# Optimization experiments

Measured on AMD Instinct MI355X. Metric: run time of the kernel, lower is better.

Reference implementation:

```python
import jax, jax.numpy as jnp
import numpy as np

N_MESH = 40962  # icosahedral level-6 mesh nodes (x[..., -40962:])


def _lin_coords(out_size, in_size, scale):
    # torch F.interpolate bilinear, align_corners=False source coords
    i = jnp.arange(out_size, dtype=jnp.float32)
    src = jnp.maximum((i + 0.5) / scale - 0.5, 0.0)
    i0 = jnp.clip(jnp.floor(src).astype(jnp.int32), 0, in_size - 1)
    i1 = jnp.minimum(i0 + 1, in_size - 1)
    w = src - i0.astype(jnp.float32)
    return i0, i1, w


def _bilinear4(x):
    # x: (B,C,H,W) -> (B,C,4H,4W), separable bilinear, align_corners=False
    B, C, H, W = x.shape
    i0, i1, wh = _lin_coords(4 * H, H, 4.0)
    x = x[:, :, i0, :] * (1.0 - wh)[None, None, :, None] + x[:, :, i1, :] * wh[None, None, :, None]
    j0, j1, ww = _lin_coords(4 * W, W, 4.0)
    x = x[:, :, :, j0] * (1.0 - ww) + x[:, :, :, j1] * ww
    return x


def _grid2mesh(x, lat, lon):
    # x: (B,C,H,W); drop last lat row, upsample x4, append broadcast pole row
    B, C, H, W = x.shape
    pole = x[:, :, -1, 0][:, :, None, None] * jnp.ones((B, C, 1, 4 * W), x.dtype)
    xi = _bilinear4(x[:, :, :-1, :])            # (B,C,4(H-1),4W)
    xi = jnp.concatenate([xi, pole], axis=2)    # (B,C,4(H-1)+1,4W)
    return xi[:, :, lat - 1, lon - 1]           # (B,C,M) gather at mesh coords


def _gcn(h, W, b, src, dst, norm, n):
    # GCNConv: sym-normalized scatter-add aggregation of linearly transformed feats
    h = h @ W                                    # (B,N,Hd)
    msg = lambda hb: jax.ops.segment_sum(hb[src] * norm[:, None], dst, num_segments=n)
    return jax.vmap(msg)(h) + b


def reference(x, edge_index, Lat, Lon, W1, b1, W2, b2, Wl, bl, Wl1, bl1):
    B, C, H, Wd = x.shape
    mesh = _grid2mesh(x, Lat, Lon)                               # (B,C,M)
    feats = jnp.concatenate([x.reshape(B, C, H * Wd), mesh], -1)  # (B,C,N)
    h = feats.transpose(0, 2, 1)                                 # (B,N,C)
    n = h.shape[1]

    # gcn_norm with self loops (edge_weight = 1)
    loops = jnp.arange(n, dtype=edge_index.dtype)
    src = jnp.concatenate([edge_index[0], loops])
    dst = jnp.concatenate([edge_index[1], loops])
    deg = jax.ops.segment_sum(jnp.ones(src.shape, h.dtype), dst, num_segments=n)
    dinv = jnp.where(deg > 0, deg ** -0.5, 0.0)
    norm = dinv[src] * dinv[dst]

    h = _gcn(h, W1, b1, src, dst, norm, n)
    h = jax.nn.gelu(h, approximate=False)
    h = _gcn(h, W2, b2, src, dst, norm, n)
    h = h[:, -N_MESH:, :]                                        # keep mesh nodes
    out = jax.nn.gelu((h @ Wl + bl) @ Wl1 + bl1, approximate=False)
    return out.transpose(0, 2, 1)                                # (B,out_ch,M)


def setup_inputs() -> dict:
    key = jax.random.key(0)
    ks = jax.random.split(key, 16)
    B, C, H, W = 1, 69, 181, 360
    HID, OUT = 256, 256
    N = H * W + N_MESH  # 106122
    E = 500000
    x = jax.random.normal(ks[0], (B, C, H, W), jnp.float32)
    edge_index = jax.random.randint(ks[1], (2, E), 0, N, dtype=jnp.int64)
    Lat = jax.random.randint(ks[2], (N_MESH,), 1, 4 * (H - 1) + 2, dtype=jnp.int64)
    Lon = jax.random.randint(ks[3], (N_MESH,), 1, 4 * W + 1, dtype=jnp.int64)
    s = 0.05
    return {
        "x": x, "edge_index": edge_index, "Lat": Lat, "Lon": Lon,
        "W1": jax.random.normal(ks[4], (C, HID), jnp.float32) * s,
        "b1": jnp.zeros((HID,), jnp.float32),
        "W2": jax.random.normal(ks[5], (HID, HID), jnp.float32) * s,
        "b2": jnp.zeros((HID,), jnp.float32),
        "Wl": jax.random.normal(ks[6], (HID, 256), jnp.float32) * s,
        "bl": jnp.zeros((256,), jnp.float32),
        "Wl1": jax.random.normal(ks[7], (256, OUT), jnp.float32) * s,
        "bl1": jnp.zeros((OUT,), jnp.float32),
    }
```

## Files before the change

### kernel.cpp

```cpp
#include <hip/hip_runtime.h>

#define NGRID 65160
#define NMESH 40962
#define NTOT  (NGRID + NMESH)
#define CIN   69
#define KPAD1 96
#define HID   256
#define HH    181
#define WWID  360
#define SCAN_BS 1024
#define NBLK_SCAN ((NTOT + SCAN_BS - 1) / SCAN_BS)

#define NT1TILES ((NTOT + 63) / 64)
#define NT1PAD   (NT1TILES * 64)
#define NT2TILES ((NMESH + 63) / 64)
#define NT2PAD   (NT2TILES * 64)

#define W1OFF  0
#define WCOFF  (96 * 256)
#define WALLK  (96 + 256)

typedef float f32x4 __attribute__((ext_vector_type(4)));
typedef _Float16 f16;
typedef _Float16 f16x2 __attribute__((ext_vector_type(2)));
typedef _Float16 f16x4 __attribute__((ext_vector_type(4)));
typedef _Float16 f16x8 __attribute__((ext_vector_type(8)));

__device__ __forceinline__ float gelu_exact(float v) {
    return 0.5f * v * (1.0f + erff(v * 0.7071067811865476f));
}

__global__ __launch_bounds__(256) void transpose_x(const float* __restrict__ x,
                                                   f16* __restrict__ h0g) {
    __shared__ float tile[96][65];
    int s0 = blockIdx.x * 64;
    int t = threadIdx.x;
#pragma unroll
    for (int i = 0; i < 24; ++i) {
        int idx = t + i * 256;
        int c = idx >> 6, s = idx & 63;
        int gs = s0 + s;
        float v = 0.f;
        if (c < CIN && gs < NGRID) v = x[(size_t)c * NGRID + gs];
        tile[c][s] = v;
    }
    __syncthreads();
#pragma unroll
    for (int i = 0; i < 12; ++i) {
        int idx = t + i * 256;
        int r = idx / 48, u = idx % 48;
        int gr = s0 + r;
        if (gr < NGRID) {
            f16x2 p;
            p.x = (f16)tile[u * 2 + 0][r];
            p.y = (f16)tile[u * 2 + 1][r];
            ((f16x2*)h0g)[(size_t)gr * 48 + u] = p;
        }
    }
}

__global__ __launch_bounds__(256) void mesh_interp(const f16* __restrict__ h0g,
                                                   const int* __restrict__ Lat,
                                                   const int* __restrict__ Lon,
                                                   f16* __restrict__ h0m) {
    int t = blockIdx.x * 256 + threadIdx.x;
    if (t >= NMESH * 48) return;
    int j = t / 48, u = t % 48;
    int la = Lat[j] - 1;
    int lo = Lon[j] - 1;
    const f16x2* g = (const f16x2*)h0g;
    f16x2 o;
    if (la == 720) {
        o = g[(size_t)(180 * WWID) * 48 + u];
    } else {
        float sh = fmaxf((la + 0.5f) * 0.25f - 0.5f, 0.0f);
        int i0 = min((int)sh, HH - 2);
        int i1 = min(i0 + 1, HH - 2);
        float wh = sh - (float)i0;
        float sw = fmaxf((lo + 0.5f) * 0.25f - 0.5f, 0.0f);
        int j0 = min((int)sw, WWID - 1);
        int j1 = min(j0 + 1, WWID - 1);
        float ww = sw - (float)j0;
        f16x2 v00 = g[(size_t)(i0 * WWID + j0) * 48 + u];
        f16x2 v10 = g[(size_t)(i1 * WWID + j0) * 48 + u];
        f16x2 v01 = g[(size_t)(i0 * WWID + j1) * 48 + u];
        f16x2 v11 = g[(size_t)(i1 * WWID + j1) * 48 + u];
        float ax = (float)v00.x + ((float)v10.x - (float)v00.x) * wh;
        float ay = (float)v00.y + ((float)v10.y - (float)v00.y) * wh;
        float bx = (float)v01.x + ((float)v11.x - (float)v01.x) * wh;
        float by = (float)v01.y + ((float)v11.y - (float)v01.y) * wh;
        o.x = (f16)(ax + (bx - ax) * ww);
        o.y = (f16)(ay + (by - ay) * ww);
    }
    ((f16x2*)h0m)[(size_t)j * 48 + u] = o;
}

__global__ void deg_init(float* __restrict__ deg, int* __restrict__ cnt) {
    int i = blockIdx.x * 256 + threadIdx.x;
    if (i < NTOT) { deg[i] = 1.0f; cnt[i] = 0; }
}
__global__ void deg_scatter(const int* __restrict__ ei, float* __restrict__ deg, int E) {
    int e = blockIdx.x * 256 + threadIdx.x;
    if (e < E) atomicAdd(&deg[ei[E + e]], 1.0f);
}

__global__ __launch_bounds__(SCAN_BS) void scan1(const float* __restrict__ deg,
                                                 float* __restrict__ dinv,
                                                 int* __restrict__ off, int* __restrict__ bsum) {
    __shared__ int s[SCAN_BS];
    int t = threadIdx.x;
    int i = blockIdx.x * SCAN_BS + t;
    int v = (i < NTOT) ? ((int)deg[i] - 1) : 0;
    if (i < NTOT) dinv[i] = 1.0f / sqrtf((float)(v + 1));
    s[t] = v; __syncthreads();
    for (int d = 1; d < SCAN_BS; d <<= 1) {
        int x = (t >= d) ? s[t - d] : 0;
        __syncthreads();
        s[t] += x;
        __syncthreads();
    }
    if (i < NTOT) off[i] = s[t] - v;
    if (t == SCAN_BS - 1) bsum[blockIdx.x] = s[t];
}
__global__ void scan2(int* __restrict__ bsum) {
    __shared__ int s[128];
    int t = threadIdx.x;
    int v = (t < NBLK_SCAN) ? bsum[t] : 0;
    s[t] = v; __syncthreads();
    for (int d = 1; d < 128; d <<= 1) {
        int x = (t >= d) ? s[t - d] : 0;
        __syncthreads();
        s[t] += x;
        __syncthreads();
    }
    if (t < NBLK_SCAN) bsum[t] = s[t] - v;
}
__global__ __launch_bounds__(SCAN_BS) void scan3(int* __restrict__ off, const int* __restrict__ bsum) {
    int i = blockIdx.x * SCAN_BS + threadIdx.x;
    if (i < NTOT) off[i] += bsum[blockIdx.x];
}

__global__ void csr_fill(const int* __restrict__ ei, const float* __restrict__ dinv,
                         const int* __restrict__ off, int* __restrict__ cnt,
                         int2* __restrict__ epk, int E) {
    int e = blockIdx.x * 256 + threadIdx.x;
    if (e >= E) return;
    int s = ei[e], d = ei[E + e];
    int pos = off[d] + atomicAdd(&cnt[d], 1);
    epk[pos] = make_int2(s, __float_as_int(dinv[s] * dinv[d]));
}

__global__ __launch_bounds__(256) void wgemm(const float* __restrict__ A,
                                             const float* __restrict__ B,
                                             float* __restrict__ C) {
    __shared__ float As[16][68];
    __shared__ float Bs[16][64];
    int r0 = blockIdx.y * 64, c0 = blockIdx.x * 64;
    int t = threadIdx.x;
    int tr = t >> 4, tc = t & 15;
    float acc[4][4] = {};
    for (int kk = 0; kk < 256; kk += 16) {
#pragma unroll
        for (int i = 0; i < 4; ++i) {
            int idx = t + i * 256;
            int r = idx >> 4, k = idx & 15;
            As[k][r] = A[(size_t)(r0 + r) * 256 + kk + k];
        }
#pragma unroll
        for (int i = 0; i < 4; ++i) {
            int idx = t + i * 256;
            int k = idx >> 6, c = idx & 63;
            Bs[k][c] = B[(size_t)(kk + k) * 256 + c0 + c];
        }
        __syncthreads();
#pragma unroll
        for (int k = 0; k < 16; ++k) {
            float a[4], b[4];
#pragma unroll
            for (int i = 0; i < 4; ++i) a[i] = As[k][tr * 4 + i];
#pragma unroll
            for (int j = 0; j < 4; ++j) b[j] = Bs[k][tc * 4 + j];
#pragma unroll
            for (int i = 0; i < 4; ++i)
#pragma unroll
                for (int j = 0; j < 4; ++j) acc[i][j] = fmaf(a[i], b[j], acc[i][j]);
        }
        __syncthreads();
    }
#pragma unroll
    for (int i = 0; i < 4; ++i)
#pragma unroll
        for (int j = 0; j < 4; ++j)
            C[(size_t)(r0 + tr * 4 + i) * 256 + c0 + tc * 4 + j] = acc[i][j];
}

__global__ __launch_bounds__(256) void bias_k(const float* __restrict__ b2,
                                              const float* __restrict__ M1,
                                              const float* __restrict__ bl,
                                              const float* __restrict__ Wl1,
                                              const float* __restrict__ bl1,
                                              float* __restrict__ bc) {
    int c = threadIdx.x;
    float acc = bl1[c];
    for (int j = 0; j < 256; ++j) {
        acc = fmaf(b2[j], M1[(size_t)j * 256 + c], acc);
        acc = fmaf(bl[j], Wl1[(size_t)j * 256 + c], acc);
    }
    bc[c] = acc;
}

__global__ void pack_f16(const float* __restrict__ W1, const float* __restrict__ Wc,
                         f16* __restrict__ wp) {
    int t = blockIdx.x * 256 + threadIdx.x;
    if (t >= WALLK * HID) return;
    int kg = t >> 8, c = t & 255;
    const float* src; int k, Kw; size_t base;
    if (kg < 96) { src = W1; k = kg;      Kw = CIN; base = W1OFF; }
    else         { src = Wc; k = kg - 96; Kw = HID; base = WCOFF; }
    float v = (k < Kw) ? src[(size_t)k * HID + c] : 0.f;
    size_t idx = base + ((((size_t)(k >> 3)) * HID + c) << 3) + (k & 7);
    wp[idx] = (f16)v;
}

__global__ __launch_bounds__(256) void agg1(const f16* __restrict__ h0,
                                            const float* __restrict__ deg,
                                            const float* __restrict__ dinv,
                                            const int* __restrict__ off,
                                            const int2* __restrict__ epk,
                                            f16* __restrict__ P0) {
    int wv = (blockIdx.x * 256 + threadIdx.x) >> 6;
    if (wv >= NT1PAD) return;
    int lane = threadIdx.x & 63;
    if (lane >= 48) return;
    int r = wv & 63, tile = wv >> 6;
    char* dst = (char*)P0 + (size_t)tile * 12288 + ((r * 192 + lane * 4) ^ ((r & 7) << 4));
    if (wv >= NTOT) { *(unsigned*)dst = 0u; return; }
    int d = wv;
    const f16x2* g = (const f16x2*)h0;
    float dv = dinv[d];
    float w2 = dv * dv;
    f16x2 v = g[(size_t)d * 48 + lane];
    float ax = w2 * (float)v.x;
    float ay = w2 * (float)v.y;
    const int2* ep = epk + off[d];
    int n = (int)deg[d] - 1;
    int p = 0;
    for (; p + 4 <= n; p += 4) {
        int2 e0 = ep[p], e1 = ep[p + 1], e2 = ep[p + 2], e3 = ep[p + 3];
        f16x2 u0 = g[(size_t)e0.x * 48 + lane];
        f16x2 u1 = g[(size_t)e1.x * 48 + lane];
        f16x2 u2 = g[(size_t)e2.x * 48 + lane];
        f16x2 u3 = g[(size_t)e3.x * 48 + lane];
        float w0 = __int_as_float(e0.y), w1 = __int_as_float(e1.y);
        float w2b = __int_as_float(e2.y), w3 = __int_as_float(e3.y);
        ax = fmaf(w0, (float)u0.x, ax); ay = fmaf(w0, (float)u0.y, ay);
        ax = fmaf(w1, (float)u1.x, ax); ay = fmaf(w1, (float)u1.y, ay);
        ax = fmaf(w2b, (float)u2.x, ax); ay = fmaf(w2b, (float)u2.y, ay);
        ax = fmaf(w3, (float)u3.x, ax); ay = fmaf(w3, (float)u3.y, ay);
    }
    for (; p < n; ++p) {
        int2 e = ep[p];
        f16x2 u = g[(size_t)e.x * 48 + lane];
        float w = __int_as_float(e.y);
        ax = fmaf(w, (float)u.x, ax);
        ay = fmaf(w, (float)u.y, ay);
    }
    f16x2 o; o.x = (f16)ax; o.y = (f16)ay;
    *(f16x2*)dst = o;
}

__global__ __launch_bounds__(256) void agg2(const f16* __restrict__ A,
                                            const float* __restrict__ deg,
                                            const float* __restrict__ dinv,
                                            const int* __restrict__ off,
                                            const int2* __restrict__ epk,
                                            f16* __restrict__ P2) {
    int wv = (blockIdx.x * 256 + threadIdx.x) >> 6;
    if (wv >= NT2PAD) return;
    int lane = threadIdx.x & 63;
    int r = wv & 63, tile = wv >> 6;
    char* dst = (char*)P2 + (size_t)tile * 32768 + ((r * 512 + lane * 8) ^ ((r & 7) << 4));
    if (wv >= NMESH) { *(unsigned long long*)dst = 0ull; return; }
    int d = NGRID + wv;
    const f16x4* g = (const f16x4*)A;
    float dv = dinv[d];
    float w2 = dv * dv;
    f16x4 v = g[(size_t)d * 64 + lane];
    float4 acc;
    acc.x = w2 * (float)v.x; acc.y = w2 * (float)v.y;
    acc.z = w2 * (float)v.z; acc.w = w2 * (float)v.w;
    const int2* ep = epk + off[d];
    int n = (int)deg[d] - 1;
    int p = 0;
    for (; p + 4 <= n; p += 4) {
        int2 e0 = ep[p], e1 = ep[p + 1], e2 = ep[p + 2], e3 = ep[p + 3];
        f16x4 u0 = g[(size_t)e0.x * 64 + lane];
        f16x4 u1 = g[(size_t)e1.x * 64 + lane];
        f16x4 u2 = g[(size_t)e2.x * 64 + lane];
        f16x4 u3 = g[(size_t)e3.x * 64 + lane];
        float w0 = __int_as_float(e0.y), w1 = __int_as_float(e1.y);
        float w2b = __int_as_float(e2.y), w3 = __int_as_float(e3.y);
        acc.x = fmaf(w0, (float)u0.x, acc.x); acc.y = fmaf(w0, (float)u0.y, acc.y);
        acc.z = fmaf(w0, (float)u0.z, acc.z); acc.w = fmaf(w0, (float)u0.w, acc.w);
        acc.x = fmaf(w1, (float)u1.x, acc.x); acc.y = fmaf(w1, (float)u1.y, acc.y);
        acc.z = fmaf(w1, (float)u1.z, acc.z); acc.w = fmaf(w1, (float)u1.w, acc.w);
        acc.x = fmaf(w2b, (float)u2.x, acc.x); acc.y = fmaf(w2b, (float)u2.y, acc.y);
        acc.z = fmaf(w2b, (float)u2.z, acc.z); acc.w = fmaf(w2b, (float)u2.w, acc.w);
        acc.x = fmaf(w3, (float)u3.x, acc.x); acc.y = fmaf(w3, (float)u3.y, acc.y);
        acc.z = fmaf(w3, (float)u3.z, acc.z); acc.w = fmaf(w3, (float)u3.w, acc.w);
    }
    for (; p < n; ++p) {
        int2 e = ep[p];
        f16x4 u = g[(size_t)e.x * 64 + lane];
        float w = __int_as_float(e.y);
        acc.x = fmaf(w, (float)u.x, acc.x); acc.y = fmaf(w, (float)u.y, acc.y);
        acc.z = fmaf(w, (float)u.z, acc.z); acc.w = fmaf(w, (float)u.w, acc.w);
    }
    f16x4 o;
    o.x = (f16)acc.x; o.y = (f16)acc.y; o.z = (f16)acc.z; o.w = (f16)acc.w;
    *(f16x4*)dst = o;
}

__global__ __launch_bounds__(256) void gemm1_f16(const f16* __restrict__ P0,
                                                 const f16* __restrict__ wp,
                                                 const float* __restrict__ bias,
                                                 f16* __restrict__ Af) {
    __shared__ __align__(16) f16 As[64 * 96];
    const int tile = blockIdx.x;
    const int row0 = tile * 64;
    const int t = threadIdx.x;
    const int lane = t & 63;
    const int wave = t >> 6;
    const int l15 = lane & 15, l4 = lane >> 4;
    const int colw = wave * 64;
    const char* src = (const char*)P0 + (size_t)tile * 12288;
#pragma unroll
    for (int i = 0; i < 3; ++i) {
        int o = t * 16 + i * 4096;
        *(uint4*)((char*)As + o) = *(const uint4*)(src + o);
    }
    __syncthreads();
    f32x4 acc[4][4] = {};
#pragma unroll
    for (int ks = 0; ks < 96; ks += 32) {
        f16x8 a[4], b[4];
#pragma unroll
        for (int rb = 0; rb < 4; ++rb) {
            int r = rb * 16 + l15;
            int byte = r * 192 + (ks + l4 * 8) * 2;
            int swz = byte ^ ((r & 7) << 4);
            a[rb] = *(f16x8*)((char*)As + swz);
        }
#pragma unroll
        for (int cb = 0; cb < 4; ++cb) {
            int c = colw + cb * 16 + l15;
            size_t off = ((((size_t)ks >> 3) + l4) * HID + c) << 3;
            b[cb] = *(const f16x8*)(wp + W1OFF + off);
        }
#pragma unroll
        for (int rb = 0; rb < 4; ++rb)
#pragma unroll
            for (int cb = 0; cb < 4; ++cb)
                acc[rb][cb] = __builtin_amdgcn_mfma_f32_16x16x32_f16(a[rb], b[cb], acc[rb][cb], 0, 0, 0);
    }
#pragma unroll
    for (int rb = 0; rb < 4; ++rb) {
#pragma unroll
        for (int r = 0; r < 4; ++r) {
            int gr = row0 + rb * 16 + l4 * 4 + r;
            if (gr < NTOT) {
#pragma unroll
                for (int cb = 0; cb < 4; ++cb) {
                    int gc = colw + cb * 16 + l15;
                    float v = acc[rb][cb][r] + bias[gc];
                    Af[(size_t)gr * HID + gc] = (f16)gelu_exact(v);
                }
            }
        }
    }
}

__global__ __launch_bounds__(256) void final_k(const f16* __restrict__ P2,
                                               const f16* __restrict__ wp,
                                               const float* __restrict__ bc,
                                               float* __restrict__ out) {
    __shared__ __align__(16) f16 Ps[64 * 256];
    const int tile = blockIdx.x;
    const int row0 = tile * 64;
    const int t = threadIdx.x;
    const int lane = t & 63;
    const int wave = t >> 6;
    const int l15 = lane & 15, l4 = lane >> 4;
    const int cw = wave * 64;
    const char* src = (const char*)P2 + (size_t)tile * 32768;
#pragma unroll
    for (int i = 0; i < 8; ++i) {
        int o = t * 16 + i * 4096;
        *(uint4*)((char*)Ps + o) = *(const uint4*)(src + o);
    }
    __syncthreads();
    f32x4 acc[4][4] = {};
#pragma unroll
    for (int ks = 0; ks < 256; ks += 32) {
        f16x8 w[4], p[4];
#pragma unroll
        for (int mb = 0; mb < 4; ++mb) {
            int c = cw + mb * 16 + l15;
            size_t off = ((((size_t)ks >> 3) + l4) * HID + c) << 3;
            w[mb] = *(const f16x8*)(wp + WCOFF + off);
        }
#pragma unroll
        for (int jb = 0; jb < 4; ++jb) {
            int r = jb * 16 + l15;
            int byte = r * 512 + (ks + l4 * 8) * 2;
            int swz = byte ^ ((r & 7) << 4);
            p[jb] = *(f16x8*)((char*)Ps + swz);
        }
#pragma unroll
        for (int mb = 0; mb < 4; ++mb)
#pragma unroll
            for (int jb = 0; jb < 4; ++jb)
                acc[mb][jb] = __builtin_amdgcn_mfma_f32_16x16x32_f16(w[mb], p[jb], acc[mb][jb], 0, 0, 0);
    }
    const bool full = (row0 + 64 <= NMESH);
#pragma unroll
    for (int mb = 0; mb < 4; ++mb) {
#pragma unroll
        for (int r = 0; r < 4; ++r) {
            int c = cw + mb * 16 + l4 * 4 + r;
            float bv = bc[c];
            float* orow = out + (size_t)c * NMESH + row0;
#pragma unroll
            for (int jb = 0; jb < 4; ++jb) {
                int j = jb * 16 + l15;
                float v = gelu_exact(acc[mb][jb][r] + bv);
                if (full || row0 + j < NMESH) orow[j] = v;
            }
        }
    }
}

extern "C" void kernel_launch(void* const* d_in, const int* in_sizes, int n_in,
                              void* d_out, int out_size, void* d_ws, size_t ws_size,
                              hipStream_t stream) {
    const float* x   = (const float*)d_in[0];
    const int*   ei  = (const int*)d_in[1];
    const int*   Lat = (const int*)d_in[2];
    const int*   Lon = (const int*)d_in[3];
    const float* W1  = (const float*)d_in[4];
    const float* b1  = (const float*)d_in[5];
    const float* W2  = (const float*)d_in[6];
    const float* b2  = (const float*)d_in[7];
    const float* Wl  = (const float*)d_in[8];
    const float* bl  = (const float*)d_in[9];
    const float* Wl1 = (const float*)d_in[10];
    const float* bl1 = (const float*)d_in[11];
    float* out = (float*)d_out;
    const int E = in_sizes[1] / 2;

    f16*   h0  = (f16*)d_out;
    int2*  epk = (int2*)((char*)d_out + (size_t)NTOT * KPAD1 * 2);

    f16*   P0   = (f16*)d_ws;
    f16*   Af   = P0 + (size_t)NT1TILES * 6144;
    f16*   P2   = Af + (size_t)NTOT * HID;
    float* deg  = (float*)(P2 + (size_t)NT2TILES * 16384);
    float* dinv = deg + NTOT;
    int*   off  = (int*)(dinv + NTOT);
    int*   cnt  = off + NTOT;
    int*   bsum = cnt + NTOT;
    float* M1   = (float*)(bsum + 128);
    float* WcF  = M1 + HID * HID;
    float* bc   = WcF + HID * HID;
    f16*   wp   = (f16*)(bc + HID);

    transpose_x<<<(NGRID + 63) / 64, 256, 0, stream>>>(x, h0);
    mesh_interp<<<(NMESH * 48 + 255) / 256, 256, 0, stream>>>(h0, Lat, Lon,
                                                              h0 + (size_t)NGRID * KPAD1);

    deg_init<<<(NTOT + 255) / 256, 256, 0, stream>>>(deg, cnt);
    deg_scatter<<<(E + 255) / 256, 256, 0, stream>>>(ei, deg, E);
    scan1<<<NBLK_SCAN, SCAN_BS, 0, stream>>>(deg, dinv, off, bsum);
    scan2<<<1, 128, 0, stream>>>(bsum);
    scan3<<<NBLK_SCAN, SCAN_BS, 0, stream>>>(off, bsum);
    csr_fill<<<(E + 255) / 256, 256, 0, stream>>>(ei, dinv, off, cnt, epk, E);

    dim3 gW(4, 4);
    wgemm<<<gW, 256, 0, stream>>>(Wl, Wl1, M1);
    wgemm<<<gW, 256, 0, stream>>>(W2, M1, WcF);
    bias_k<<<1, 256, 0, stream>>>(b2, M1, bl, Wl1, bl1, bc);
    pack_f16<<<(WALLK * HID + 255) / 256, 256, 0, stream>>>(W1, WcF, wp);

    agg1<<<(int)(((long long)NT1PAD * 64 + 255) / 256), 256, 0, stream>>>(
        h0, deg, dinv, off, epk, P0);
    gemm1_f16<<<NT1TILES, 256, 0, stream>>>(P0, wp, b1, Af);

    agg2<<<(int)(((long long)NT2PAD * 64 + 255) / 256), 256, 0, stream>>>(
        Af, deg, dinv, off, epk, P2);

    final_k<<<NT2TILES, 256, 0, stream>>>(P2, wp, bc, out);
}
```

Baseline: 257.2 us.

## Vectorize hidden-layer stores and stage final output through LDS for coalesced writes

The first GEMM epilogue now packs four f16 outputs per lane into one vector store. This permutes the column order of the intermediate features, and the packed Wc weight rows are permuted to match. The final kernel no longer writes strided scalar outputs. It stages GELU results in padded LDS in two channel halves, then writes coalesced float4 rows of the channel-major output. This adds extra barriers and LDS traffic, and the float4 stores rely on dword-aligned (not 16-byte aligned) global addresses since NMESH is not a multiple of 4.

```diff
diff --git a/kernel.cpp b/kernel.cpp
--- a/kernel.cpp
+++ b/kernel.cpp
@@ -214,11 +214,17 @@
     int t = blockIdx.x * 256 + threadIdx.x;
     if (t >= WALLK * HID) return;
     int kg = t >> 8, c = t & 255;
-    const float* src; int k, Kw; size_t base;
-    if (kg < 96) { src = W1; k = kg;      Kw = CIN; base = W1OFF; }
-    else         { src = Wc; k = kg - 96; Kw = HID; base = WCOFF; }
-    float v = (k < Kw) ? src[(size_t)k * HID + c] : 0.f;
-    size_t idx = base + ((((size_t)(k >> 3)) * HID + c) << 3) + (k & 7);
+    float v;
+    size_t idx;
+    if (kg < 96) {
+        v = (kg < CIN) ? W1[(size_t)kg * HID + c] : 0.f;
+        idx = W1OFF + ((((size_t)(kg >> 3)) * HID + c) << 3) + (kg & 7);
+    } else {
+        int ks = kg - 96;
+        int kl = (ks & ~63) + ((ks & 3) << 4) + ((ks & 63) >> 2);
+        v = Wc[(size_t)kl * HID + c];
+        idx = WCOFF + ((((size_t)(ks >> 3)) * HID + c) << 3) + (ks & 7);
+    }
     wp[idx] = (f16)v;
 }
 
@@ -369,12 +375,14 @@
         for (int r = 0; r < 4; ++r) {
             int gr = row0 + rb * 16 + l4 * 4 + r;
             if (gr < NTOT) {
+                f16x4 o;
 #pragma unroll
                 for (int cb = 0; cb < 4; ++cb) {
                     int gc = colw + cb * 16 + l15;
                     float v = acc[rb][cb][r] + bias[gc];
-                    Af[(size_t)gr * HID + gc] = (f16)gelu_exact(v);
+                    o[cb] = (f16)gelu_exact(v);
                 }
+                *(f16x4*)(Af + (size_t)gr * HID + colw + l15 * 4) = o;
             }
         }
     }
@@ -384,7 +392,9 @@
                                                const f16* __restrict__ wp,
                                                const float* __restrict__ bc,
                                                float* __restrict__ out) {
-    __shared__ __align__(16) f16 Ps[64 * 256];
+    __shared__ __align__(16) char smem[64 * 132 * 4];
+    f16* Ps = (f16*)smem;
+    float* lf = (float*)smem;
     const int tile = blockIdx.x;
     const int row0 = tile * 64;
     const int t = threadIdx.x;
@@ -423,18 +433,48 @@
                 acc[mb][jb] = __builtin_amdgcn_mfma_f32_16x16x32_f16(w[mb], p[jb], acc[mb][jb], 0, 0, 0);
     }
     const bool full = (row0 + 64 <= NMESH);
-#pragma unroll
-    for (int mb = 0; mb < 4; ++mb) {
-#pragma unroll
-        for (int r = 0; r < 4; ++r) {
-            int c = cw + mb * 16 + l4 * 4 + r;
-            float bv = bc[c];
-            float* orow = out + (size_t)c * NMESH + row0;
-#pragma unroll
-            for (int jb = 0; jb < 4; ++jb) {
-                int j = jb * 16 + l15;
-                float v = gelu_exact(acc[mb][jb][r] + bv);
-                if (full || row0 + j < NMESH) orow[j] = v;
+    for (int ph = 0; ph < 2; ++ph) {
+        __syncthreads();
+        if ((wave >> 1) == ph) {
+            int cbase = cw & 127;
+#pragma unroll
+            for (int mb = 0; mb < 4; ++mb) {
+                int chl = cbase + mb * 16 + l4 * 4;
+                int c = cw + mb * 16 + l4 * 4;
+                float b0 = bc[c + 0], b1v = bc[c + 1], b2v = bc[c + 2], b3v = bc[c + 3];
+#pragma unroll
+                for (int jb = 0; jb < 4; ++jb) {
+                    int j = jb * 16 + l15;
+                    float4 o;
+                    o.x = gelu_exact(acc[mb][jb][0] + b0);
+                    o.y = gelu_exact(acc[mb][jb][1] + b1v);
+                    o.z = gelu_exact(acc[mb][jb][2] + b2v);
+                    o.w = gelu_exact(acc[mb][jb][3] + b3v);
+                    *(float4*)&lf[j * 132 + chl] = o;
+                }
+            }
+        }
+        __syncthreads();
+        if (full) {
+#pragma unroll
+            for (int i = 0; i < 8; ++i) {
+                int id = t + i * 256;
+                int chl = id >> 4, n0 = (id & 15) * 4;
+                float4 v;
+                v.x = lf[(n0 + 0) * 132 + chl];
+                v.y = lf[(n0 + 1) * 132 + chl];
+                v.z = lf[(n0 + 2) * 132 + chl];
+                v.w = lf[(n0 + 3) * 132 + chl];
+                *(float4*)(out + (size_t)(ph * 128 + chl) * NMESH + row0 + n0) = v;
+            }
+        } else {
+            for (int i = 0; i < 8; ++i) {
+                int id = t + i * 256;
+                int chl = id >> 4, n0 = (id & 15) * 4;
+                for (int k2 = 0; k2 < 4; ++k2)
+                    if (row0 + n0 + k2 < NMESH)
+                        out[(size_t)(ph * 128 + chl) * NMESH + row0 + n0 + k2] =
+                            lf[(n0 + k2) * 132 + chl];
             }
         }
     }
```

Result: slower. 271.7 us (+5.7%).

## Permute hidden layout so gemm1 waves write 16-byte rows without LDS staging

Applied to the files above, without the earlier changes.

gemm1 is restructured so each wave computes a full 16x256 output strip. It reads its A fragments straight from the pre-swizzled P0 buffer instead of staging a tile in shared memory behind a barrier. Each lane now owns 16 contiguous hidden columns, so the GELU output is written as two 16-byte vector stores instead of many scattered 2-byte stores. To keep results correct, the hidden feature order is permuted, and pack_f16 permutes the rows of the next-layer weight Wc to match. The trade-offs are 16 accumulator vectors per wave, which raises register pressure, and weight fragments that are no longer shared across row blocks within a workgroup.

```diff
diff --git a/kernel.cpp b/kernel.cpp
--- a/kernel.cpp
+++ b/kernel.cpp
@@ -214,11 +214,17 @@
     int t = blockIdx.x * 256 + threadIdx.x;
     if (t >= WALLK * HID) return;
     int kg = t >> 8, c = t & 255;
-    const float* src; int k, Kw; size_t base;
-    if (kg < 96) { src = W1; k = kg;      Kw = CIN; base = W1OFF; }
-    else         { src = Wc; k = kg - 96; Kw = HID; base = WCOFF; }
-    float v = (k < Kw) ? src[(size_t)k * HID + c] : 0.f;
-    size_t idx = base + ((((size_t)(k >> 3)) * HID + c) << 3) + (k & 7);
+    float v;
+    size_t idx;
+    if (kg < 96) {
+        v = (kg < CIN) ? W1[(size_t)kg * HID + c] : 0.f;
+        idx = W1OFF + ((((size_t)(kg >> 3)) * HID + c) << 3) + (kg & 7);
+    } else {
+        int ks = kg - 96;
+        int kl = ((ks & 15) << 4) | (ks >> 4);
+        v = Wc[(size_t)kl * HID + c];
+        idx = WCOFF + ((((size_t)(ks >> 3)) * HID + c) << 3) + (ks & 7);
+    }
     wp[idx] = (f16)v;
 }
 
@@ -325,57 +331,55 @@
                                                  const f16* __restrict__ wp,
                                                  const float* __restrict__ bias,
                                                  f16* __restrict__ Af) {
-    __shared__ __align__(16) f16 As[64 * 96];
-    const int tile = blockIdx.x;
-    const int row0 = tile * 64;
-    const int t = threadIdx.x;
-    const int lane = t & 63;
-    const int wave = t >> 6;
+    const int wid = (blockIdx.x * 256 + threadIdx.x) >> 6;
+    const int lane = threadIdx.x & 63;
     const int l15 = lane & 15, l4 = lane >> 4;
-    const int colw = wave * 64;
-    const char* src = (const char*)P0 + (size_t)tile * 12288;
-#pragma unroll
-    for (int i = 0; i < 3; ++i) {
-        int o = t * 16 + i * 4096;
-        *(uint4*)((char*)As + o) = *(const uint4*)(src + o);
-    }
-    __syncthreads();
-    f32x4 acc[4][4] = {};
-#pragma unroll
-    for (int ks = 0; ks < 96; ks += 32) {
-        f16x8 a[4], b[4];
-#pragma unroll
-        for (int rb = 0; rb < 4; ++rb) {
-            int r = rb * 16 + l15;
-            int byte = r * 192 + (ks + l4 * 8) * 2;
-            int swz = byte ^ ((r & 7) << 4);
-            a[rb] = *(f16x8*)((char*)As + swz);
-        }
-#pragma unroll
-        for (int cb = 0; cb < 4; ++cb) {
-            int c = colw + cb * 16 + l15;
-            size_t off = ((((size_t)ks >> 3) + l4) * HID + c) << 3;
-            b[cb] = *(const f16x8*)(wp + W1OFF + off);
-        }
-#pragma unroll
-        for (int rb = 0; rb < 4; ++rb)
-#pragma unroll
-            for (int cb = 0; cb < 4; ++cb)
-                acc[rb][cb] = __builtin_amdgcn_mfma_f32_16x16x32_f16(a[rb], b[cb], acc[rb][cb], 0, 0, 0);
-    }
-#pragma unroll
-    for (int rb = 0; rb < 4; ++rb) {
-#pragma unroll
-        for (int r = 0; r < 4; ++r) {
-            int gr = row0 + rb * 16 + l4 * 4 + r;
-            if (gr < NTOT) {
-#pragma unroll
-                for (int cb = 0; cb < 4; ++cb) {
-                    int gc = colw + cb * 16 + l15;
-                    float v = acc[rb][cb][r] + bias[gc];
-                    Af[(size_t)gr * HID + gc] = (f16)gelu_exact(v);
-                }
-            }
+    const int tile = wid >> 2, rb = wid & 3;
+
+    f16x8 a[3];
+    {
+        const char* base = (const char*)P0 + (size_t)tile * 12288;
+        int r = rb * 16 + l15;
+#pragma unroll
+        for (int ks = 0; ks < 3; ++ks) {
+            int byte = r * 192 + (ks * 32 + l4 * 8) * 2;
+            a[ks] = *(const f16x8*)(base + (byte ^ ((r & 7) << 4)));
+        }
+    }
+
+    f32x4 acc[16];
+#pragma unroll
+    for (int cb = 0; cb < 16; ++cb) acc[cb] = (f32x4)0.f;
+#pragma unroll
+    for (int cb = 0; cb < 16; ++cb) {
+        int c = cb * 16 + l15;
+#pragma unroll
+        for (int ks = 0; ks < 3; ++ks) {
+            size_t o = ((((size_t)ks << 2) + l4) * HID + c) << 3;
+            f16x8 w = *(const f16x8*)(wp + W1OFF + o);
+            acc[cb] = __builtin_amdgcn_mfma_f32_16x16x32_f16(a[ks], w, acc[cb], 0, 0, 0);
+        }
+    }
+
+    float bv[16];
+#pragma unroll
+    for (int cb = 0; cb < 16; ++cb) bv[cb] = bias[cb * 16 + l15];
+
+    const int gr0 = tile * 64 + rb * 16 + l4 * 4;
+#pragma unroll
+    for (int reg = 0; reg < 4; ++reg) {
+        int gr = gr0 + reg;
+        if (gr < NTOT) {
+            f16x8 lo, hi;
+#pragma unroll
+            for (int cb = 0; cb < 8; ++cb)
+                lo[cb] = (f16)gelu_exact(acc[cb][reg] + bv[cb]);
+#pragma unroll
+            for (int cb = 8; cb < 16; ++cb)
+                hi[cb - 8] = (f16)gelu_exact(acc[cb][reg] + bv[cb]);
+            f16* dst = Af + (size_t)gr * HID + l15 * 16;
+            *(f16x8*)dst = lo;
+            *(f16x8*)(dst + 8) = hi;
         }
     }
 }
```

Measured after the change: 260.5 us. No clear change (+1.3%).
